# Kernel optimization log

Hardware: AMD Instinct MI355X
Metric: run time of the kernel (lower is better)

Reference implementation:

```python
import jax, jax.numpy as jnp
import numpy as np

D = 1024      # model dim
DH = 64       # dim_head
H = 8         # heads
INNER = DH * H
L = 6         # depth
NL = 64       # num_latents
MF = 128      # max_num_frames
FF = 4 * D    # ff_mult * dim
B, T, F, V = 4, 8, 4, 256


def _ln(x, g, b):
    m = x.mean(-1, keepdims=True)
    v = x.var(-1, keepdims=True)
    return (x - m) / jnp.sqrt(v + 1e-5) * g + b


def setup_inputs() -> dict:
    key = jax.random.key(0)
    ks = jax.random.split(key, 8)
    s = 0.02
    x = jax.random.normal(ks[0], (B, T, F, V, D), jnp.float32)
    latents = jax.random.normal(ks[1], (NL, D), jnp.float32)
    frame_embs = jax.random.normal(ks[2], (MF, D), jnp.float32)
    Wq = jax.random.normal(ks[3], (L, D, INNER), jnp.float32) * s
    Wkv = jax.random.normal(ks[4], (L, D, 2 * INNER), jnp.float32) * s
    Wo = jax.random.normal(ks[5], (L, INNER, D), jnp.float32) * s
    W1 = jax.random.normal(ks[6], (L, D, FF), jnp.float32) * s
    W2 = jax.random.normal(ks[7], (L, FF, D), jnp.float32) * s
    ones = jnp.ones((L, D), jnp.float32)
    zeros = jnp.zeros((L, D), jnp.float32)
    return dict(
        x=x, latents=latents, frame_embs=frame_embs,
        g_media=ones, b_media=zeros, g_lat=ones, b_lat=zeros,
        Wq=Wq, Wkv=Wkv, Wo=Wo, g_ff=ones, b_ff=zeros, W1=W1, W2=W2,
        g_out=jnp.ones((D,), jnp.float32), b_out=jnp.zeros((D,), jnp.float32),
    )


def reference(x, latents, frame_embs, g_media, b_media, g_lat, b_lat,
              Wq, Wkv, Wo, g_ff, b_ff, W1, W2, g_out, b_out):
    scale = DH ** -0.5
    # add frame embeddings (indexed by T, as in original code), merge F,v dims
    x = x + frame_embs[:T][None, :, None, None, :]
    x = x.reshape(B, T, F * V, D)
    lat0 = jnp.broadcast_to(latents, (B, T, NL, D))

    def split_heads(a):  # (b, t, n, h*d) -> (b, h, t, n, d)
        return a.reshape(B, T, -1, H, DH).transpose(0, 3, 1, 2, 4)

    def block(lat, p):
        gm, bm, gl, bl, wq, wkv, wo, gf, bf, w1, w2 = p
        xm = _ln(x, gm, bm)
        ln_l = _ln(lat, gl, bl)
        q = (ln_l @ wq) * scale
        kv = jnp.concatenate([xm, ln_l], axis=-2) @ wkv
        k, v = jnp.split(kv, 2, axis=-1)
        q, k, v = split_heads(q), split_heads(k), split_heads(v)
        sim = jnp.einsum('bhtid,bhtjd->bhtij', q, k)
        attn = jax.nn.softmax(sim, axis=-1)
        o = jnp.einsum('bhtij,bhtjd->bhtid', attn, v)
        o = o.transpose(0, 2, 3, 1, 4).reshape(B, T, NL, INNER)
        lat = o @ wo + lat
        ff = jax.nn.gelu(_ln(lat, gf, bf) @ w1, approximate=False) @ w2
        return lat + ff, None

    lat, _ = jax.lax.scan(block, lat0,
                          (g_media, b_media, g_lat, b_lat, Wq, Wkv, Wo,
                           g_ff, b_ff, W1, W2))
    return _ln(lat, g_out, b_out)
```

## Files before the change

### kernel.cpp

```cpp
#include <hip/hip_runtime.h>
#include <math.h>

#define D_      1024
#define DH_     64
#define H_      8
#define INNER_  512
#define L_      6
#define NL_     64
#define FF_     4096
#define B_      4
#define T_      8
#define FV_     1024
#define BT_     32
#define MROWS_  32768
#define NKV_    1088
#define KVROWS_ 34816
#define ZB_     256

typedef __bf16 bf16;
typedef __bf16 bf16x8 __attribute__((ext_vector_type(8)));
typedef __bf16 bf16x4 __attribute__((ext_vector_type(4)));
typedef float  f32x4  __attribute__((ext_vector_type(4)));

#define BARRIER() { asm volatile("" ::: "memory"); __builtin_amdgcn_s_barrier(); asm volatile("" ::: "memory"); }
#define ENDPH() { __builtin_amdgcn_sched_barrier(0); asm volatile("s_waitcnt lgkmcnt(0)"); __builtin_amdgcn_sched_barrier(0); BARRIER(); }

__device__ __forceinline__ void gload_lds16(const bf16* g, bf16* l) {
    __builtin_amdgcn_global_load_lds(
        (const __attribute__((address_space(1))) unsigned int*)g,
        (__attribute__((address_space(3))) unsigned int*)l, 16, 0, 0);
}

__device__ __forceinline__ float wred_sum(float v) {
#pragma unroll
    for (int o = 32; o > 0; o >>= 1) v += __shfl_xor(v, o, 64);
    return v;
}

__device__ __forceinline__ float gelu_f(float x) {
    return 0.5f * x * (1.0f + erff(x * 0.70710678118654752440f));
}

__global__ __launch_bounds__(256) void xhat_k(const float* __restrict__ x,
                                              const float* __restrict__ fe,
                                              bf16* __restrict__ xhat) {
    __shared__ float red[8];
    int row = blockIdx.x;
    int t = (row >> 10) & 7;
    const float* xr = x + (size_t)row * D_;
    const float* fr_ = fe + (size_t)t * D_;
    int tid = threadIdx.x, c = tid * 4;
    float4 v = *(const float4*)(xr + c);
    float4 f = *(const float4*)(fr_ + c);
    v.x += f.x; v.y += f.y; v.z += f.z; v.w += f.w;
    float s = v.x + v.y + v.z + v.w;
    float ss = v.x * v.x + v.y * v.y + v.z * v.z + v.w * v.w;
    s = wred_sum(s); ss = wred_sum(ss);
    if ((tid & 63) == 0) { red[tid >> 6] = s; red[4 + (tid >> 6)] = ss; }
    __syncthreads();
    s = red[0] + red[1] + red[2] + red[3];
    ss = red[4] + red[5] + red[6] + red[7];
    float mean = s * (1.0f / D_);
    float rstd = rsqrtf(ss * (1.0f / D_) - mean * mean + 1e-5f);
    bf16x4 o;
    o[0] = (bf16)((v.x - mean) * rstd);
    o[1] = (bf16)((v.y - mean) * rstd);
    o[2] = (bf16)((v.z - mean) * rstd);
    o[3] = (bf16)((v.w - mean) * rstd);
    *(bf16x4*)(xhat + (size_t)row * D_ + c) = o;
}

__global__ __launch_bounds__(256) void latinit_k(const float* __restrict__ latents,
                                                 float* __restrict__ lat) {
    int row = blockIdx.x;
    int i = row & 63;
    int c = threadIdx.x * 4;
    float4 v = *(const float4*)(latents + (size_t)i * D_ + c);
    *(float4*)(lat + (size_t)row * D_ + c) = v;
}

template<int OUTF>
__global__ __launch_bounds__(256) void ln_k(const float* __restrict__ in,
                                            const float* __restrict__ g,
                                            const float* __restrict__ b,
                                            void* __restrict__ out) {
    __shared__ float red[8];
    int row = blockIdx.x;
    const float* x = in + (size_t)row * D_;
    int tid = threadIdx.x, c = tid * 4;
    float4 v = *(const float4*)(x + c);
    float s = v.x + v.y + v.z + v.w;
    float ss = v.x * v.x + v.y * v.y + v.z * v.z + v.w * v.w;
    s = wred_sum(s); ss = wred_sum(ss);
    if ((tid & 63) == 0) { red[tid >> 6] = s; red[4 + (tid >> 6)] = ss; }
    __syncthreads();
    s = red[0] + red[1] + red[2] + red[3];
    ss = red[4] + red[5] + red[6] + red[7];
    float mean = s * (1.0f / D_);
    float rstd = rsqrtf(ss * (1.0f / D_) - mean * mean + 1e-5f);
    float4 gv = *(const float4*)(g + c);
    float4 bv = *(const float4*)(b + c);
    float o0 = (v.x - mean) * rstd * gv.x + bv.x;
    float o1 = (v.y - mean) * rstd * gv.y + bv.y;
    float o2 = (v.z - mean) * rstd * gv.z + bv.z;
    float o3 = (v.w - mean) * rstd * gv.w + bv.w;
    if (OUTF) {
        *(float4*)((float*)out + (size_t)row * D_ + c) = make_float4(o0, o1, o2, o3);
    } else {
        bf16x4 o; o[0] = (bf16)o0; o[1] = (bf16)o1; o[2] = (bf16)o2; o[3] = (bf16)o3;
        *(bf16x4*)((bf16*)out + (size_t)row * D_ + c) = o;
    }
}

template<int NP, int OUTF>
__global__ __launch_bounds__(256) void accln_k(float* __restrict__ lat,
                                               const float* __restrict__ p, long long s,
                                               const float* __restrict__ g,
                                               const float* __restrict__ b,
                                               void* __restrict__ out) {
    __shared__ float red[8];
    int row = blockIdx.x;
    int tid = threadIdx.x, c = tid * 4;
    float* lr = lat + (size_t)row * D_;
    float4 a = *(const float4*)(lr + c);
#pragma unroll
    for (int w = 0; w < NP; w++) {
        float4 x = *(const float4*)(p + (size_t)w * s + (size_t)row * D_ + c);
        a.x += x.x; a.y += x.y; a.z += x.z; a.w += x.w;
    }
    if (!OUTF) *(float4*)(lr + c) = a;
    float sm = a.x + a.y + a.z + a.w;
    float ss = a.x * a.x + a.y * a.y + a.z * a.z + a.w * a.w;
    sm = wred_sum(sm); ss = wred_sum(ss);
    if ((tid & 63) == 0) { red[tid >> 6] = sm; red[4 + (tid >> 6)] = ss; }
    __syncthreads();
    sm = red[0] + red[1] + red[2] + red[3];
    ss = red[4] + red[5] + red[6] + red[7];
    float mean = sm * (1.0f / D_);
    float rstd = rsqrtf(ss * (1.0f / D_) - mean * mean + 1e-5f);
    float4 gv = *(const float4*)(g + c);
    float4 bv = *(const float4*)(b + c);
    float o0 = (a.x - mean) * rstd * gv.x + bv.x;
    float o1 = (a.y - mean) * rstd * gv.y + bv.y;
    float o2 = (a.z - mean) * rstd * gv.z + bv.z;
    float o3 = (a.w - mean) * rstd * gv.w + bv.w;
    if (OUTF) {
        *(float4*)((float*)out + (size_t)row * D_ + c) = make_float4(o0, o1, o2, o3);
    } else {
        bf16x4 o; o[0] = (bf16)o0; o[1] = (bf16)o1; o[2] = (bf16)o2; o[3] = (bf16)o3;
        *(bf16x4*)((bf16*)out + (size_t)row * D_ + c) = o;
    }
}

__device__ __forceinline__ void wt_tile(const float* __restrict__ in, int R, int C,
                                        bf16* __restrict__ out, int bx, int by,
                                        const float* __restrict__ sc,
                                        const float* __restrict__ bm,
                                        float* __restrict__ bkv) {
    __shared__ float t[32][33];
    int c0 = bx * 32, r0 = by * 32;
    int tx = threadIdx.x & 31, ty = threadIdx.x >> 5;
#pragma unroll
    for (int i = 0; i < 4; i++)
        t[ty + i * 8][tx] = in[(size_t)(r0 + ty + i * 8) * C + c0 + tx];
    __syncthreads();
    float scale = sc ? sc[r0 + tx] : 1.0f;
#pragma unroll
    for (int i = 0; i < 4; i++)
        out[(size_t)(c0 + ty + i * 8) * R + r0 + tx] = (bf16)(t[tx][ty + i * 8] * scale);
    if (bm && ty == 0) {
        float s = 0.0f;
#pragma unroll
        for (int r = 0; r < 32; r++) s += bm[r0 + r] * t[r][tx];
        atomicAdd(&bkv[c0 + tx], s);
    }
}

__global__ __launch_bounds__(256) void wprep_all(const float* __restrict__ Wq,
                                                 const float* __restrict__ Wkv,
                                                 const float* __restrict__ Wo,
                                                 const float* __restrict__ W1,
                                                 const float* __restrict__ W2,
                                                 const float* __restrict__ g_media,
                                                 const float* __restrict__ b_media,
                                                 float* __restrict__ bkv6,
                                                 bf16* __restrict__ Bcat6,
                                                 bf16* __restrict__ WkvTg6,
                                                 bf16* __restrict__ WoT6,
                                                 bf16* __restrict__ W1T6,
                                                 bf16* __restrict__ W2T6) {
    int l = blockIdx.x / 11264;
    int id = blockIdx.x - l * 11264;
    const float* wq  = Wq + (size_t)l * D_ * INNER_;
    const float* wkv = Wkv + (size_t)l * D_ * 2 * INNER_;
    const float* wo  = Wo + (size_t)l * INNER_ * D_;
    const float* w1  = W1 + (size_t)l * D_ * FF_;
    const float* w2  = W2 + (size_t)l * FF_ * D_;
    bf16* BcatQ  = Bcat6 + (size_t)l * 1536 * D_;
    bf16* BcatKV = BcatQ + (size_t)512 * D_;
    bf16* WkvTg  = WkvTg6 + (size_t)l * D_ * D_;
    bf16* WoT    = WoT6 + (size_t)l * D_ * INNER_;
    bf16* W1T    = W1T6 + (size_t)l * FF_ * D_;
    bf16* W2T    = W2T6 + (size_t)l * D_ * FF_;
    const float* gm = g_media + (size_t)l * D_;
    const float* bm = b_media + (size_t)l * D_;
    float* bkv = bkv6 + (size_t)l * 1024;
    if (id < 512)            wt_tile(wq, D_, INNER_, BcatQ, id & 15, id >> 4, nullptr, nullptr, nullptr);
    else if (id < 1536)  { int i = id - 512;  wt_tile(wkv, D_, 2 * INNER_, BcatKV, i & 31, i >> 5, nullptr, nullptr, nullptr); }
    else if (id < 2560)  { int i = id - 1536; wt_tile(wkv, D_, 2 * INNER_, WkvTg, i & 31, i >> 5, gm, bm, bkv); }
    else if (id < 3072)  { int i = id - 2560; wt_tile(wo, INNER_, D_, WoT, i & 31, i >> 5, nullptr, nullptr, nullptr); }
    else if (id < 7168)  { int i = id - 3072; wt_tile(w1, D_, FF_, W1T, i & 127, i >> 7, nullptr, nullptr, nullptr); }
    else                 { int i = id - 7168; wt_tile(w2, FF_, D_, W2T, i & 31, i >> 5, nullptr, nullptr, nullptr); }
}

__global__ __launch_bounds__(512, 1) void gemm_kv(const bf16* __restrict__ Ag,
                                                  const bf16* __restrict__ Bg,
                                                  bf16* __restrict__ KVb,
                                                  bf16* __restrict__ vt,
                                                  const float* __restrict__ bias) {
    __shared__ bf16 lds[2][32768];
    const int lda = D_, ldb = D_;
    const int tid = threadIdx.x;
    const int w = tid >> 6, lane = tid & 63;
    const int wm = w >> 2, wn = w & 3;
    const size_t m0 = (size_t)blockIdx.x * 256;
    const size_t n0 = (size_t)blockIdx.y * 256;
    const int nt = 16;

    const int p0 = (w * 2) * 64 + lane, p1 = p0 + 64;
    const int sr0 = p0 >> 3, sk0 = ((p0 & 7) ^ (sr0 & 7)) * 8;
    const int sr1 = p1 >> 3, sk1 = ((p1 & 7) ^ (sr1 & 7)) * 8;
    const int scw0 = (w * 2) * 512, scw1 = scw0 + 512;

    auto STAGE = [&](const bf16* g, int ld, size_t row0, int k0, bf16* bufb, int rb) {
        gload_lds16(g + (row0 + sr0) * (size_t)ld + k0 + sk0, bufb + rb + scw0);
        gload_lds16(g + (row0 + sr1) * (size_t)ld + k0 + sk1, bufb + rb + scw1);
    };

    const int fr = lane & 15;
    const int pK0 = (((lane >> 4)) ^ (fr & 7)) * 8;
    const int pK1 = ((4 + (lane >> 4)) ^ (fr & 7)) * 8;
    const size_t aoff = (size_t)(wm * 128 + fr) * 64;
    const size_t boff = 16384 + (size_t)(wn * 64 + fr) * 64;

    f32x4 acc[8][4];
#pragma unroll
    for (int i = 0; i < 8; i++)
#pragma unroll
        for (int j = 0; j < 4; j++)
#pragma unroll
            for (int r = 0; r < 4; r++) acc[i][j][r] = 0.0f;

    STAGE(Bg, ldb, n0,       0, lds[0], 16384);
    STAGE(Bg, ldb, n0 + 128, 0, lds[0], 24576);
    STAGE(Ag, lda, m0,       0, lds[0], 0);
    STAGE(Ag, lda, m0 + 128, 0, lds[0], 8192);
    STAGE(Bg, ldb, n0,       64, lds[1], 16384);
    STAGE(Bg, ldb, n0 + 128, 64, lds[1], 24576);
    STAGE(Ag, lda, m0,       64, lds[1], 0);
    asm volatile("s_waitcnt vmcnt(6)");
    BARRIER();

    for (int t = 0; t < nt; ++t) {
        const bf16* lb = lds[t & 1];
        bf16* lbw = lds[t & 1];
        bf16* lbn = lds[(t + 1) & 1];
        const int kt1 = (t + 1) << 6, kt2 = (t + 2) << 6;
        bf16x8 bfr[4][2];

        {
#pragma unroll
            for (int j = 0; j < 4; j++) {
                bfr[j][0] = *(const bf16x8*)(lb + boff + j * 1024 + pK0);
                bfr[j][1] = *(const bf16x8*)(lb + boff + j * 1024 + pK1);
            }
            bf16x8 a00 = *(const bf16x8*)(lb + aoff + 0 * 1024 + pK0);
            bf16x8 a01 = *(const bf16x8*)(lb + aoff + 0 * 1024 + pK1);
            bf16x8 a10 = *(const bf16x8*)(lb + aoff + 1 * 1024 + pK0);
            bf16x8 a11 = *(const bf16x8*)(lb + aoff + 1 * 1024 + pK1);
            if (t + 1 < nt) STAGE(Ag, lda, m0 + 128, kt1, lbn, 8192);
            BARRIER();
            asm volatile("s_waitcnt lgkmcnt(0)");
            __builtin_amdgcn_s_setprio(1);
#pragma unroll
            for (int j = 0; j < 4; j++) {
                acc[0][j] = __builtin_amdgcn_mfma_f32_16x16x32_bf16(a00, bfr[j][0], acc[0][j], 0, 0, 0);
                acc[0][j] = __builtin_amdgcn_mfma_f32_16x16x32_bf16(a01, bfr[j][1], acc[0][j], 0, 0, 0);
                acc[1][j] = __builtin_amdgcn_mfma_f32_16x16x32_bf16(a10, bfr[j][0], acc[1][j], 0, 0, 0);
                acc[1][j] = __builtin_amdgcn_mfma_f32_16x16x32_bf16(a11, bfr[j][1], acc[1][j], 0, 0, 0);
            }
            __builtin_amdgcn_s_setprio(0);
            BARRIER();
        }
        {
            bf16x8 a00 = *(const bf16x8*)(lb + aoff + 2 * 1024 + pK0);
            bf16x8 a01 = *(const bf16x8*)(lb + aoff + 2 * 1024 + pK1);
            bf16x8 a10 = *(const bf16x8*)(lb + aoff + 3 * 1024 + pK0);
            bf16x8 a11 = *(const bf16x8*)(lb + aoff + 3 * 1024 + pK1);
            if (t + 2 < nt) STAGE(Bg, ldb, n0, kt2, lbw, 16384);
            BARRIER();
            asm volatile("s_waitcnt lgkmcnt(0)");
            __builtin_amdgcn_s_setprio(1);
#pragma unroll
            for (int j = 0; j < 4; j++) {
                acc[2][j] = __builtin_amdgcn_mfma_f32_16x16x32_bf16(a00, bfr[j][0], acc[2][j], 0, 0, 0);
                acc[2][j] = __builtin_amdgcn_mfma_f32_16x16x32_bf16(a01, bfr[j][1], acc[2][j], 0, 0, 0);
                acc[3][j] = __builtin_amdgcn_mfma_f32_16x16x32_bf16(a10, bfr[j][0], acc[3][j], 0, 0, 0);
                acc[3][j] = __builtin_amdgcn_mfma_f32_16x16x32_bf16(a11, bfr[j][1], acc[3][j], 0, 0, 0);
            }
            __builtin_amdgcn_s_setprio(0);
            BARRIER();
        }
        {
            bf16x8 a00 = *(const bf16x8*)(lb + aoff + 4 * 1024 + pK0);
            bf16x8 a01 = *(const bf16x8*)(lb + aoff + 4 * 1024 + pK1);
            bf16x8 a10 = *(const bf16x8*)(lb + aoff + 5 * 1024 + pK0);
            bf16x8 a11 = *(const bf16x8*)(lb + aoff + 5 * 1024 + pK1);
            if (t + 2 < nt) STAGE(Bg, ldb, n0 + 128, kt2, lbw, 24576);
            BARRIER();
            asm volatile("s_waitcnt lgkmcnt(0)");
            __builtin_amdgcn_s_setprio(1);
#pragma unroll
            for (int j = 0; j < 4; j++) {
                acc[4][j] = __builtin_amdgcn_mfma_f32_16x16x32_bf16(a00, bfr[j][0], acc[4][j], 0, 0, 0);
                acc[4][j] = __builtin_amdgcn_mfma_f32_16x16x32_bf16(a01, bfr[j][1], acc[4][j], 0, 0, 0);
                acc[5][j] = __builtin_amdgcn_mfma_f32_16x16x32_bf16(a10, bfr[j][0], acc[5][j], 0, 0, 0);
                acc[5][j] = __builtin_amdgcn_mfma_f32_16x16x32_bf16(a11, bfr[j][1], acc[5][j], 0, 0, 0);
            }
            __builtin_amdgcn_s_setprio(0);
            BARRIER();
        }
        {
            bf16x8 a00 = *(const bf16x8*)(lb + aoff + 6 * 1024 + pK0);
            bf16x8 a01 = *(const bf16x8*)(lb + aoff + 6 * 1024 + pK1);
            bf16x8 a10 = *(const bf16x8*)(lb + aoff + 7 * 1024 + pK0);
            bf16x8 a11 = *(const bf16x8*)(lb + aoff + 7 * 1024 + pK1);
            if (t + 2 < nt) STAGE(Ag, lda, m0, kt2, lbw, 0);
            BARRIER();
            asm volatile("s_waitcnt lgkmcnt(0)");
            __builtin_amdgcn_s_setprio(1);
#pragma unroll
            for (int j = 0; j < 4; j++) {
                acc[6][j] = __builtin_amdgcn_mfma_f32_16x16x32_bf16(a00, bfr[j][0], acc[6][j], 0, 0, 0);
                acc[6][j] = __builtin_amdgcn_mfma_f32_16x16x32_bf16(a01, bfr[j][1], acc[6][j], 0, 0, 0);
                acc[7][j] = __builtin_amdgcn_mfma_f32_16x16x32_bf16(a10, bfr[j][0], acc[7][j], 0, 0, 0);
                acc[7][j] = __builtin_amdgcn_mfma_f32_16x16x32_bf16(a11, bfr[j][1], acc[7][j], 0, 0, 0);
            }
            __builtin_amdgcn_s_setprio(0);
            if (t < nt - 2)       { asm volatile("s_waitcnt vmcnt(6)"); }
            else if (t == nt - 2) { asm volatile("s_waitcnt vmcnt(0)"); }
            BARRIER();
        }
    }

    const int fq = (lane >> 4) * 4;
#pragma unroll
    for (int i = 0; i < 8; i++)
#pragma unroll
        for (int j = 0; j < 4; j++) {
            size_t cb = n0 + wn * 64 + j * 16 + fr;
            float bv = bias[cb];
            size_t mb = m0 + wm * 128 + i * 16 + fq;
            if (cb < 512) {
#pragma unroll
                for (int r = 0; r < 4; r++) {
                    size_t m = mb + r;
                    size_t rb = m + ((m >> 10) << 6);
                    KVb[rb * 512 + cb] = (bf16)(acc[i][j][r] + bv);
                }
            } else {
                int hh = ((int)cb - 512) >> 6, dh = ((int)cb - 512) & 63;
                size_t bt = mb >> 10, jl = mb & 1023;
                bf16x4 v4;
#pragma unroll
                for (int r = 0; r < 4; r++) v4[r] = (bf16)(acc[i][j][r] + bv);
                *(bf16x4*)(vt + ((bt * 8 + hh) * 64 + dh) * (size_t)NKV_ + jl) = v4;
            }
        }
}

template<int MODE>
__global__ __launch_bounds__(512, 1) void gemm_ff(const bf16* __restrict__ Ag, int lda,
                                                  const bf16* __restrict__ Bg, int ldb,
                                                  void* __restrict__ C, int ldc,
                                                  int K, long long czs) {
    __shared__ bf16 lds[2][24576];
    const int tid = threadIdx.x;
    const int w = tid >> 6, lane = tid & 63;
    const int wm = w >> 2, wn = w & 3;
    const size_t m0 = (size_t)blockIdx.x * 128;
    const size_t n0 = (size_t)blockIdx.y * 256;
    const int klen = K / gridDim.z;
    const int koff = blockIdx.z * klen;
    const int nt = klen >> 6;

    const int p0 = (w * 2) * 64 + lane, p1 = p0 + 64;
    const int sr0 = p0 >> 3, sk0 = ((p0 & 7) ^ (sr0 & 7)) * 8;
    const int sr1 = p1 >> 3, sk1 = ((p1 & 7) ^ (sr1 & 7)) * 8;
    const int scw0 = (w * 2) * 512, scw1 = scw0 + 512;

    auto STAGE = [&](const bf16* g, int ld, size_t row0, int k0, bf16* bufb, int rb) {
        gload_lds16(g + (row0 + sr0) * (size_t)ld + k0 + sk0, bufb + rb + scw0);
        gload_lds16(g + (row0 + sr1) * (size_t)ld + k0 + sk1, bufb + rb + scw1);
    };

    const int fr = lane & 15;
    const int pK0 = (((lane >> 4)) ^ (fr & 7)) * 8;
    const int pK1 = ((4 + (lane >> 4)) ^ (fr & 7)) * 8;
    const size_t aoff = (size_t)(wm * 64 + fr) * 64;
    const size_t boff = 8192 + (size_t)(wn * 64 + fr) * 64;

    f32x4 acc[4][4];
#pragma unroll
    for (int i = 0; i < 4; i++)
#pragma unroll
        for (int j = 0; j < 4; j++)
#pragma unroll
            for (int r = 0; r < 4; r++) acc[i][j][r] = 0.0f;

    bf16x8 aX[2], aY[2], bA[4][2], bB[4][2];

    auto LDA1 = [&](const bf16* lb, int i0, bf16x8 (&d)[2]) {
        d[0] = *(const bf16x8*)(lb + aoff + (size_t)i0 * 1024 + pK0);
        d[1] = *(const bf16x8*)(lb + aoff + (size_t)i0 * 1024 + pK1);
    };
    auto LDB8 = [&](const bf16* lb, bf16x8 (&bb)[4][2]) {
#pragma unroll
        for (int j = 0; j < 4; j++) {
            bb[j][0] = *(const bf16x8*)(lb + boff + j * 1024 + pK0);
            bb[j][1] = *(const bf16x8*)(lb + boff + j * 1024 + pK1);
        }
    };
    auto MM1 = [&](int i0, bf16x8 (&a)[2], bf16x8 (&bb)[4][2]) {
        __builtin_amdgcn_s_setprio(1);
#pragma unroll
        for (int j = 0; j < 4; j++) {
            acc[i0][j] = __builtin_amdgcn_mfma_f32_16x16x32_bf16(a[0], bb[j][0], acc[i0][j], 0, 0, 0);
            acc[i0][j] = __builtin_amdgcn_mfma_f32_16x16x32_bf16(a[1], bb[j][1], acc[i0][j], 0, 0, 0);
        }
        __builtin_amdgcn_s_setprio(0);
    };

    STAGE(Ag, lda, m0,       koff,      lds[0], 0);
    STAGE(Bg, ldb, n0,       koff,      lds[0], 8192);
    STAGE(Bg, ldb, n0 + 128, koff,      lds[0], 16384);
    STAGE(Bg, ldb, n0,       koff + 64, lds[1], 8192);
    STAGE(Bg, ldb, n0 + 128, koff + 64, lds[1], 16384);
    asm volatile("s_waitcnt vmcnt(4)");
    BARRIER();
    LDB8(lds[0], bA);
    LDA1(lds[0], 0, aX);

    auto tile4 = [&](const bf16* lb, bf16* lbn, bf16x8 (&BU)[4][2], bf16x8 (&BL)[4][2], int t) {
        bf16* lbw = (bf16*)lb;
        LDA1(lb, 1, aY);
        if (t + 1 < nt) STAGE(Ag, lda, m0, koff + ((t + 1) << 6), lbn, 0);
        MM1(0, aX, BU);
        ENDPH();
        LDA1(lb, 2, aX);
        if (t + 2 < nt) STAGE(Bg, ldb, n0, koff + ((t + 2) << 6), lbw, 8192);
        MM1(1, aY, BU);
        ENDPH();
        LDA1(lb, 3, aY);
        if (t + 2 < nt) STAGE(Bg, ldb, n0 + 128, koff + ((t + 2) << 6), lbw, 16384);
        MM1(2, aX, BU);
        __builtin_amdgcn_sched_barrier(0);
        asm volatile("s_waitcnt lgkmcnt(0)");
        __builtin_amdgcn_sched_barrier(0);
        if (t < nt - 2)       { asm volatile("s_waitcnt vmcnt(4)"); }
        else if (t == nt - 2) { asm volatile("s_waitcnt vmcnt(0)"); }
        BARRIER();
        if (t + 1 < nt) { LDB8(lbn, BL); LDA1(lbn, 0, aX); }
        MM1(3, aY, BU);
        ENDPH();
    };

    for (int t = 0; t < nt; t += 2) {
        tile4(lds[0], lds[1], bA, bB, t);
        tile4(lds[1], lds[0], bB, bA, t + 1);
    }

    const int fq = (lane >> 4) * 4;
#pragma unroll
    for (int i = 0; i < 4; i++)
#pragma unroll
        for (int j = 0; j < 4; j++) {
            size_t cb = n0 + wn * 64 + j * 16 + fr;
            size_t mb = m0 + wm * 64 + i * 16 + fq;
#pragma unroll
            for (int r = 0; r < 4; r++) {
                float v = acc[i][j][r];
                if (MODE == 4) {
                    ((float*)C + blockIdx.z * czs)[(mb + r) * (size_t)ldc + cb] = v;
                } else {
                    ((bf16*)C)[(mb + r) * (size_t)ldc + cb] = (bf16)gelu_f(v);
                }
            }
        }
}

template<int MODE, int CMAP>
__global__ __launch_bounds__(256) void gemm128(const bf16* __restrict__ A, int lda,
                                               const bf16* __restrict__ Bw, int ldb,
                                               void* __restrict__ C, int ldc,
                                               int K, float scale,
                                               long long czs, void* __restrict__ C2,
                                               void* __restrict__ C3) {
    __shared__ bf16 As[128 * 32];
    __shared__ bf16 Bs[128 * 32];
    const int tid = threadIdx.x;
    const int wave = tid >> 6;
    const int lane = tid & 63;
    const size_t m0 = (size_t)blockIdx.x * 128;
    const size_t n0 = (size_t)blockIdx.y * 128;
    const int wm = (wave >> 1) * 64;
    const int wn = (wave & 1) * 64;

    const int klen = K / gridDim.z;
    const int koff = blockIdx.z * klen;

    const int r0 = tid >> 2;
    const int c0 = ((tid & 3) ^ ((tid >> 3) & 3)) * 8;
    const bf16* ga0 = A + (m0 + r0) * lda + c0 + koff;
    const bf16* ga1 = A + (m0 + r0 + 64) * lda + c0 + koff;
    const bf16* gb0 = Bw + (n0 + r0) * ldb + c0 + koff;
    const bf16* gb1 = Bw + (n0 + r0 + 64) * ldb + c0 + koff;
    bf16* la0 = As + wave * 512;
    bf16* la1 = As + 2048 + wave * 512;
    bf16* lb0 = Bs + wave * 512;
    bf16* lb1 = Bs + 2048 + wave * 512;

    f32x4 acc[4][4];
#pragma unroll
    for (int i = 0; i < 4; i++)
#pragma unroll
        for (int j = 0; j < 4; j++)
#pragma unroll
            for (int r = 0; r < 4; r++) acc[i][j][r] = 0.0f;

    const int fr = lane & 15;
    const int q = lane >> 4;
    const int sw = (q ^ ((fr >> 1) & 3)) * 8;

    for (int kt = 0; kt < klen; kt += 32) {
        gload_lds16(ga0 + kt, la0);
        gload_lds16(ga1 + kt, la1);
        gload_lds16(gb0 + kt, lb0);
        gload_lds16(gb1 + kt, lb1);
        __syncthreads();
        bf16x8 af[4], bfv[4];
#pragma unroll
        for (int i = 0; i < 4; i++) {
            af[i]  = *(const bf16x8*)(As + (wm + i * 16 + fr) * 32 + sw);
            bfv[i] = *(const bf16x8*)(Bs + (wn + i * 16 + fr) * 32 + sw);
        }
#pragma unroll
        for (int i = 0; i < 4; i++)
#pragma unroll
            for (int j = 0; j < 4; j++)
                acc[i][j] = __builtin_amdgcn_mfma_f32_16x16x32_bf16(af[i], bfv[j], acc[i][j], 0, 0, 0);
        __syncthreads();
    }

    const int fq = (lane >> 4) * 4;
#pragma unroll
    for (int i = 0; i < 4; i++)
#pragma unroll
        for (int j = 0; j < 4; j++) {
            size_t cb = n0 + wn + j * 16 + fr;
            size_t mb = m0 + wm + i * 16 + fq;
            if (CMAP == 3) {
                if (cb < 512) {
#pragma unroll
                    for (int r = 0; r < 4; r++)
                        ((bf16*)C)[(mb + r) * 512 + cb] = (bf16)(acc[i][j][r] * scale);
                } else if (cb < 1024) {
#pragma unroll
                    for (int r = 0; r < 4; r++) {
                        size_t m = mb + r;
                        size_t rb = (m >> 6) * (size_t)NKV_ + 1024 + (m & 63);
                        ((bf16*)C2)[rb * 512 + (cb - 512)] = (bf16)acc[i][j][r];
                    }
                } else {
                    int hh = ((int)cb - 1024) >> 6, dh = ((int)cb - 1024) & 63;
                    size_t bt = mb >> 6, jl = 1024 + (mb & 63);
                    bf16x4 v4;
#pragma unroll
                    for (int r = 0; r < 4; r++) v4[r] = (bf16)acc[i][j][r];
                    *(bf16x4*)((bf16*)C3 + ((bt * 8 + hh) * 64 + dh) * (size_t)NKV_ + jl) = v4;
                }
            } else {
#pragma unroll
                for (int r = 0; r < 4; r++) {
                    float v = acc[i][j][r];
                    if (MODE == 4) {
                        ((float*)C + blockIdx.z * czs)[(mb + r) * ldc + cb] = v;
                    } else {
                        ((bf16*)C)[(mb + r) * ldc + cb] = (bf16)v;
                    }
                }
            }
        }
}

__global__ __launch_bounds__(256, 2) void attn_k(const bf16* __restrict__ qb,
                                                 const bf16* __restrict__ KVb,
                                                 const bf16* __restrict__ vt,
                                                 float* __restrict__ partO,
                                                 float* __restrict__ partML) {
    __shared__ float comb[4][64 * 66];
    __shared__ float sc[4][64];
    __shared__ float mw[4][64], lw[4][64];
    const int bid = blockIdx.x;
    const int z = bid >> 1, half = bid & 1;
    const int bt = z >> 3, h = z & 7;
    const int tid = threadIdx.x, w = tid >> 6, lane = tid & 63;
    const int fr = lane & 15, g = lane >> 4;
    const bf16* Qz = qb + (size_t)(bt * 64) * INNER_ + h * DH_;
    const bf16* Kz = KVb + (size_t)bt * NKV_ * 512 + h * DH_;
    const bf16* Vz = vt + (size_t)z * (DH_ * NKV_);
    bf16* Pw = (bf16*)(&comb[w][0]);

    bf16x8 qf[4][2];
#pragma unroll
    for (int nj = 0; nj < 4; nj++)
#pragma unroll
        for (int ks = 0; ks < 2; ks++)
            qf[nj][ks] = *(const bf16x8*)(Qz + (size_t)(fr + 16 * nj) * INNER_ + g * 8 + ks * 32);

    f32x4 acc_o[4][4];
#pragma unroll
    for (int i = 0; i < 4; i++)
#pragma unroll
        for (int j = 0; j < 4; j++)
#pragma unroll
            for (int r = 0; r < 4; r++) acc_o[i][j][r] = 0.0f;
    float m_reg[4] = {-INFINITY, -INFINITY, -INFINITY, -INFINITY};
    float l_reg[4] = {0.0f, 0.0f, 0.0f, 0.0f};

    const int cbase = half ? 9 : 0;
    const int nch = half ? 2 : ((w == 0) ? 3 : 2);
    for (int ci = 0; ci < nch; ci++) {
        const int kc0 = (cbase + w + ci * 4) * 64;
        f32x4 s[4][4];
#pragma unroll
        for (int i = 0; i < 4; i++)
#pragma unroll
            for (int j = 0; j < 4; j++)
#pragma unroll
                for (int r = 0; r < 4; r++) s[i][j][r] = 0.0f;
#pragma unroll
        for (int ks = 0; ks < 2; ks++) {
            bf16x8 kf[4];
#pragma unroll
            for (int mi = 0; mi < 4; mi++)
                kf[mi] = *(const bf16x8*)(Kz + (size_t)(kc0 + fr + 16 * mi) * 512 + g * 8 + ks * 32);
#pragma unroll
            for (int mi = 0; mi < 4; mi++)
#pragma unroll
                for (int nj = 0; nj < 4; nj++)
                    s[mi][nj] = __builtin_amdgcn_mfma_f32_16x16x32_bf16(kf[mi], qf[nj][ks], s[mi][nj], 0, 0, 0);
        }
        float pmax[4];
#pragma unroll
        for (int nj = 0; nj < 4; nj++) {
            float mx = s[0][nj][0];
#pragma unroll
            for (int mi = 0; mi < 4; mi++)
#pragma unroll
                for (int r = 0; r < 4; r++) mx = fmaxf(mx, s[mi][nj][r]);
            mx = fmaxf(mx, __shfl_xor(mx, 16, 64));
            mx = fmaxf(mx, __shfl_xor(mx, 32, 64));
            pmax[nj] = mx;
        }
        bool big = (pmax[0] > m_reg[0] + 8.0f) || (pmax[1] > m_reg[1] + 8.0f) ||
                   (pmax[2] > m_reg[2] + 8.0f) || (pmax[3] > m_reg[3] + 8.0f);
        if (__any(big ? 1 : 0)) {
            float so[4];
#pragma unroll
            for (int nj = 0; nj < 4; nj++) {
                float mn = fmaxf(m_reg[nj], pmax[nj]);
                so[nj] = __expf(m_reg[nj] - mn);
                m_reg[nj] = mn;
                l_reg[nj] *= so[nj];
            }
            if (g == 0) {
#pragma unroll
                for (int nj = 0; nj < 4; nj++) sc[w][fr + 16 * nj] = so[nj];
            }
            asm volatile("s_waitcnt lgkmcnt(0)" ::: "memory");
#pragma unroll
            for (int mi = 0; mi < 4; mi++)
#pragma unroll
                for (int r = 0; r < 4; r++) {
                    float sq = sc[w][16 * mi + 4 * g + r];
#pragma unroll
                    for (int jd = 0; jd < 4; jd++) acc_o[mi][jd][r] *= sq;
                }
        }
        float psum[4] = {0.0f, 0.0f, 0.0f, 0.0f};
#pragma unroll
        for (int mi = 0; mi < 4; mi++)
#pragma unroll
            for (int nj = 0; nj < 4; nj++) {
                bf16x4 pb4;
#pragma unroll
                for (int r = 0; r < 4; r++) {
                    float pv = __expf(s[mi][nj][r] - m_reg[nj]);
                    psum[nj] += pv;
                    pb4[r] = (bf16)pv;
                }
                *(bf16x4*)(Pw + (size_t)(fr + 16 * nj) * 72 + 16 * mi + 4 * g) = pb4;
            }
#pragma unroll
        for (int nj = 0; nj < 4; nj++) {
            float ps = psum[nj];
            ps += __shfl_xor(ps, 16, 64);
            ps += __shfl_xor(ps, 32, 64);
            l_reg[nj] += ps;
        }
        asm volatile("s_waitcnt lgkmcnt(0)" ::: "memory");
#pragma unroll
        for (int ks = 0; ks < 2; ks++) {
            bf16x8 af[4], vf[4];
#pragma unroll
            for (int mi = 0; mi < 4; mi++)
                af[mi] = *(const bf16x8*)(Pw + (size_t)(fr + 16 * mi) * 72 + g * 8 + ks * 32);
#pragma unroll
            for (int jd = 0; jd < 4; jd++)
                vf[jd] = *(const bf16x8*)(Vz + (size_t)(fr + 16 * jd) * NKV_ + kc0 + g * 8 + ks * 32);
#pragma unroll
            for (int mi = 0; mi < 4; mi++)
#pragma unroll
                for (int jd = 0; jd < 4; jd++)
                    acc_o[mi][jd] = __builtin_amdgcn_mfma_f32_16x16x32_bf16(af[mi], vf[jd], acc_o[mi][jd], 0, 0, 0);
        }
    }

    if (g == 0) {
#pragma unroll
        for (int nj = 0; nj < 4; nj++) {
            mw[w][fr + 16 * nj] = m_reg[nj];
            lw[w][fr + 16 * nj] = l_reg[nj];
        }
    }
    asm volatile("s_waitcnt lgkmcnt(0)" ::: "memory");
#pragma unroll
    for (int mi = 0; mi < 4; mi++)
#pragma unroll
        for (int jd = 0; jd < 4; jd++)
#pragma unroll
            for (int r = 0; r < 4; r++)
                comb[w][(16 * mi + 4 * g + r) * 66 + fr + 16 * jd] = acc_o[mi][jd][r];
    __syncthreads();
    {
        int q = tid >> 2, d0 = (tid & 3) * 16;
        float M = fmaxf(fmaxf(mw[0][q], mw[1][q]), fmaxf(mw[2][q], mw[3][q]));
        float al[4], l = 0.0f;
#pragma unroll
        for (int ww = 0; ww < 4; ww++) { al[ww] = __expf(mw[ww][q] - M); l += al[ww] * lw[ww][q]; }
        float* pO = partO + (size_t)bid * 4096 + q * 64 + d0;
#pragma unroll
        for (int dd = 0; dd < 16; dd++) {
            float o = 0.0f;
#pragma unroll
            for (int ww = 0; ww < 4; ww++) o += comb[ww][q * 66 + d0 + dd] * al[ww];
            pO[dd] = o;
        }
        if ((tid & 3) == 0) {
            partML[bid * 128 + q] = M;
            partML[bid * 128 + 64 + q] = l;
        }
    }
}

__global__ __launch_bounds__(256) void attn_comb(const float* __restrict__ partO,
                                                 const float* __restrict__ partML,
                                                 bf16* __restrict__ ob) {
    int z = blockIdx.x, bt = z >> 3, h = z & 7;
    int tid = threadIdx.x, q = tid >> 2, d0 = (tid & 3) * 16;
    int b0 = z * 2, b1 = z * 2 + 1;
    float M0 = partML[b0 * 128 + q], l0 = partML[b0 * 128 + 64 + q];
    float M1 = partML[b1 * 128 + q], l1 = partML[b1 * 128 + 64 + q];
    float M = fmaxf(M0, M1);
    float a0 = __expf(M0 - M), a1 = __expf(M1 - M);
    float inv = 1.0f / (a0 * l0 + a1 * l1);
    const float* pO0 = partO + (size_t)b0 * 4096 + q * 64 + d0;
    const float* pO1 = partO + (size_t)b1 * 4096 + q * 64 + d0;
    bf16 outv[16];
#pragma unroll
    for (int dd = 0; dd < 16; dd++)
        outv[dd] = (bf16)((a0 * pO0[dd] + a1 * pO1[dd]) * inv);
    bf16* dst = ob + (size_t)(bt * 64 + q) * INNER_ + h * 64 + d0;
    *(bf16x8*)dst = *(bf16x8*)outv;
    *(bf16x8*)(dst + 8) = *(bf16x8*)(outv + 8);
}

extern "C" void kernel_launch(void* const* d_in, const int* in_sizes, int n_in,
                              void* d_out, int out_size, void* d_ws, size_t ws_size,
                              hipStream_t stream) {
    const float* x       = (const float*)d_in[0];
    const float* latents = (const float*)d_in[1];
    const float* fe      = (const float*)d_in[2];
    const float* g_media = (const float*)d_in[3];
    const float* b_media = (const float*)d_in[4];
    const float* g_lat   = (const float*)d_in[5];
    const float* b_lat   = (const float*)d_in[6];
    const float* Wq      = (const float*)d_in[7];
    const float* Wkv     = (const float*)d_in[8];
    const float* Wo      = (const float*)d_in[9];
    const float* g_ff    = (const float*)d_in[10];
    const float* b_ff    = (const float*)d_in[11];
    const float* W1      = (const float*)d_in[12];
    const float* W2      = (const float*)d_in[13];
    const float* g_out   = (const float*)d_in[14];
    const float* b_out   = (const float*)d_in[15];

    char* p = (char*)d_ws;
    auto alloc = [&](size_t bytes) { char* r = p; p += (bytes + 255) & ~(size_t)255; return r; };
    bf16*  xhat  = (bf16*)alloc((size_t)MROWS_ * D_ * 2);
    float* lat   = (float*)alloc((size_t)2048 * D_ * 4);
    bf16*  lnl   = (bf16*)alloc((size_t)2048 * D_ * 2);
    bf16*  qb    = (bf16*)alloc((size_t)2048 * INNER_ * 2);
    bf16*  KVb   = (bf16*)alloc((size_t)KVROWS_ * 512 * 2);
    bf16*  vt    = (bf16*)alloc((size_t)ZB_ * DH_ * NKV_ * 2);
    bf16*  ob    = (bf16*)alloc((size_t)2048 * INNER_ * 2);
    bf16*  Bcat6 = (bf16*)alloc((size_t)L_ * 1536 * D_ * 2);
    bf16*  WkvTg6= (bf16*)alloc((size_t)L_ * D_ * D_ * 2);
    bf16*  WoT6  = (bf16*)alloc((size_t)L_ * D_ * INNER_ * 2);
    bf16*  W1T6  = (bf16*)alloc((size_t)L_ * FF_ * D_ * 2);
    bf16*  W2T6  = (bf16*)alloc((size_t)L_ * D_ * FF_ * 2);
    float* bkv6  = (float*)alloc((size_t)L_ * 1024 * 4);
    float* ffp   = (float*)alloc((size_t)4 * 2048 * D_ * 4);
    bf16*  ffh   = vt;
    float* partO = ffp;
    float* partML= ffp + (size_t)512 * 4096;

    xhat_k<<<MROWS_, 256, 0, stream>>>(x, fe, xhat);
    latinit_k<<<2048, 256, 0, stream>>>(latents, lat);
    ln_k<0><<<2048, 256, 0, stream>>>(lat, g_lat, b_lat, lnl);
    hipMemsetAsync(bkv6, 0, (size_t)L_ * 1024 * 4, stream);
    wprep_all<<<L_ * 11264, 256, 0, stream>>>(Wq, Wkv, Wo, W1, W2, g_media, b_media,
                                              bkv6, Bcat6, WkvTg6, WoT6, W1T6, W2T6);

    const long long PS = (long long)2048 * D_;

    for (int l = 0; l < L_; l++) {
        const float* gf = g_ff + (size_t)l * D_;
        const float* bf_ = b_ff + (size_t)l * D_;
        bf16* Bcat  = Bcat6 + (size_t)l * 1536 * D_;
        bf16* WkvTg = WkvTg6 + (size_t)l * D_ * D_;
        bf16* WoT   = WoT6 + (size_t)l * D_ * INNER_;
        bf16* W1T   = W1T6 + (size_t)l * FF_ * D_;
        bf16* W2T   = W2T6 + (size_t)l * D_ * FF_;
        float* bkv  = bkv6 + (size_t)l * 1024;

        gemm_kv<<<dim3(128, 4), 512, 0, stream>>>(xhat, WkvTg, KVb, vt, bkv);
        gemm128<0, 3><<<dim3(16, 12), 256, 0, stream>>>(
            lnl, D_, Bcat, D_, qb, 0, D_, 0.125f, 0, KVb, vt);

        attn_k<<<2 * ZB_, 256, 0, stream>>>(qb, KVb, vt, partO, partML);
        attn_comb<<<ZB_, 256, 0, stream>>>(partO, partML, ob);

        gemm128<4, 0><<<dim3(16, 8, 2), 256, 0, stream>>>(
            ob, INNER_, WoT, INNER_, ffp, D_, INNER_, 1.0f, PS, nullptr, nullptr);
        accln_k<2, 0><<<2048, 256, 0, stream>>>(lat, ffp, PS, gf, bf_, lnl);

        gemm_ff<3><<<dim3(16, 16), 512, 0, stream>>>(
            lnl, D_, W1T, D_, ffh, FF_, D_, 0);
        gemm_ff<4><<<dim3(16, 4, 4), 512, 0, stream>>>(
            ffh, FF_, W2T, FF_, ffp, D_, FF_, PS);
        if (l < L_ - 1) {
            accln_k<4, 0><<<2048, 256, 0, stream>>>(lat, ffp, PS,
                g_lat + (size_t)(l + 1) * D_, b_lat + (size_t)(l + 1) * D_, lnl);
        } else {
            accln_k<4, 1><<<2048, 256, 0, stream>>>(lat, ffp, PS, g_out, b_out, (float*)d_out);
        }
    }
}
```

Before: 1.330 ms.

## Merge split-KV attention into single pass and use 64x64 weight-transpose tiles

The attention kernel no longer splits each (bt,h) across two blocks with a separate combine kernel. Each block now walks all 17 KV chunks across its four waves and normalises and writes bf16 output directly, which removes the partial-output round trip through global memory and one launch per layer. The price is half as many blocks (256) for attention, so fewer CUs are busy. Separately, the weight-prep transpose goes from 32x32 to 64x64 tiles, which cuts the block count fourfold but uses more LDS per block.

```diff
diff --git a/kernel.cpp b/kernel.cpp
--- a/kernel.cpp
+++ b/kernel.cpp
@@ -152,26 +152,26 @@
     }
 }
 
-__device__ __forceinline__ void wt_tile(const float* __restrict__ in, int R, int C,
-                                        bf16* __restrict__ out, int bx, int by,
-                                        const float* __restrict__ sc,
-                                        const float* __restrict__ bm,
-                                        float* __restrict__ bkv) {
-    __shared__ float t[32][33];
-    int c0 = bx * 32, r0 = by * 32;
-    int tx = threadIdx.x & 31, ty = threadIdx.x >> 5;
-#pragma unroll
-    for (int i = 0; i < 4; i++)
-        t[ty + i * 8][tx] = in[(size_t)(r0 + ty + i * 8) * C + c0 + tx];
+__device__ __forceinline__ void wt_tile64(const float* __restrict__ in, int R, int C,
+                                          bf16* __restrict__ out, int bx, int by,
+                                          const float* __restrict__ sc,
+                                          const float* __restrict__ bm,
+                                          float* __restrict__ bkv) {
+    __shared__ float t[64][65];
+    int c0 = bx * 64, r0 = by * 64;
+    int tx = threadIdx.x & 63, ty = threadIdx.x >> 6;
+#pragma unroll
+    for (int i = 0; i < 16; i++)
+        t[ty + i * 4][tx] = in[(size_t)(r0 + ty + i * 4) * C + c0 + tx];
     __syncthreads();
     float scale = sc ? sc[r0 + tx] : 1.0f;
 #pragma unroll
-    for (int i = 0; i < 4; i++)
-        out[(size_t)(c0 + ty + i * 8) * R + r0 + tx] = (bf16)(t[tx][ty + i * 8] * scale);
+    for (int i = 0; i < 16; i++)
+        out[(size_t)(c0 + ty + i * 4) * R + r0 + tx] = (bf16)(t[tx][ty + i * 4] * scale);
     if (bm && ty == 0) {
         float s = 0.0f;
 #pragma unroll
-        for (int r = 0; r < 32; r++) s += bm[r0 + r] * t[r][tx];
+        for (int r = 0; r < 64; r++) s += bm[r0 + r] * t[r][tx];
         atomicAdd(&bkv[c0 + tx], s);
     }
 }
@@ -189,8 +189,8 @@
                                                  bf16* __restrict__ WoT6,
                                                  bf16* __restrict__ W1T6,
                                                  bf16* __restrict__ W2T6) {
-    int l = blockIdx.x / 11264;
-    int id = blockIdx.x - l * 11264;
+    int l = blockIdx.x / 2816;
+    int id = blockIdx.x - l * 2816;
     const float* wq  = Wq + (size_t)l * D_ * INNER_;
     const float* wkv = Wkv + (size_t)l * D_ * 2 * INNER_;
     const float* wo  = Wo + (size_t)l * INNER_ * D_;
@@ -205,12 +205,12 @@
     const float* gm = g_media + (size_t)l * D_;
     const float* bm = b_media + (size_t)l * D_;
     float* bkv = bkv6 + (size_t)l * 1024;
-    if (id < 512)            wt_tile(wq, D_, INNER_, BcatQ, id & 15, id >> 4, nullptr, nullptr, nullptr);
-    else if (id < 1536)  { int i = id - 512;  wt_tile(wkv, D_, 2 * INNER_, BcatKV, i & 31, i >> 5, nullptr, nullptr, nullptr); }
-    else if (id < 2560)  { int i = id - 1536; wt_tile(wkv, D_, 2 * INNER_, WkvTg, i & 31, i >> 5, gm, bm, bkv); }
-    else if (id < 3072)  { int i = id - 2560; wt_tile(wo, INNER_, D_, WoT, i & 31, i >> 5, nullptr, nullptr, nullptr); }
-    else if (id < 7168)  { int i = id - 3072; wt_tile(w1, D_, FF_, W1T, i & 127, i >> 7, nullptr, nullptr, nullptr); }
-    else                 { int i = id - 7168; wt_tile(w2, FF_, D_, W2T, i & 31, i >> 5, nullptr, nullptr, nullptr); }
+    if (id < 128)            wt_tile64(wq, D_, INNER_, BcatQ, id & 7, id >> 3, nullptr, nullptr, nullptr);
+    else if (id < 384)   { int i = id - 128;  wt_tile64(wkv, D_, 2 * INNER_, BcatKV, i & 15, i >> 4, nullptr, nullptr, nullptr); }
+    else if (id < 640)   { int i = id - 384;  wt_tile64(wkv, D_, 2 * INNER_, WkvTg, i & 15, i >> 4, gm, bm, bkv); }
+    else if (id < 768)   { int i = id - 640;  wt_tile64(wo, INNER_, D_, WoT, i & 15, i >> 4, nullptr, nullptr, nullptr); }
+    else if (id < 1792)  { int i = id - 768;  wt_tile64(w1, D_, FF_, W1T, i & 63, i >> 6, nullptr, nullptr, nullptr); }
+    else                 { int i = id - 1792; wt_tile64(w2, FF_, D_, W2T, i & 15, i >> 4, nullptr, nullptr, nullptr); }
 }
 
 __global__ __launch_bounds__(512, 1) void gemm_kv(const bf16* __restrict__ Ag,
@@ -606,14 +606,11 @@
 __global__ __launch_bounds__(256, 2) void attn_k(const bf16* __restrict__ qb,
                                                  const bf16* __restrict__ KVb,
                                                  const bf16* __restrict__ vt,
-                                                 float* __restrict__ partO,
-                                                 float* __restrict__ partML) {
+                                                 bf16* __restrict__ ob) {
     __shared__ float comb[4][64 * 66];
     __shared__ float sc[4][64];
     __shared__ float mw[4][64], lw[4][64];
-    const int bid = blockIdx.x;
-    const int z = bid >> 1, half = bid & 1;
-    const int bt = z >> 3, h = z & 7;
+    const int z = blockIdx.x, bt = z >> 3, h = z & 7;
     const int tid = threadIdx.x, w = tid >> 6, lane = tid & 63;
     const int fr = lane & 15, g = lane >> 4;
     const bf16* Qz = qb + (size_t)(bt * 64) * INNER_ + h * DH_;
@@ -638,10 +635,9 @@
     float m_reg[4] = {-INFINITY, -INFINITY, -INFINITY, -INFINITY};
     float l_reg[4] = {0.0f, 0.0f, 0.0f, 0.0f};
 
-    const int cbase = half ? 9 : 0;
-    const int nch = half ? 2 : ((w == 0) ? 3 : 2);
+    const int nch = (w == 0) ? 5 : 4;
     for (int ci = 0; ci < nch; ci++) {
-        const int kc0 = (cbase + w + ci * 4) * 64;
+        const int kc0 = (w + ci * 4) * 64;
         f32x4 s[4][4];
 #pragma unroll
         for (int i = 0; i < 4; i++)
@@ -759,41 +755,19 @@
         float al[4], l = 0.0f;
 #pragma unroll
         for (int ww = 0; ww < 4; ww++) { al[ww] = __expf(mw[ww][q] - M); l += al[ww] * lw[ww][q]; }
-        float* pO = partO + (size_t)bid * 4096 + q * 64 + d0;
+        float inv = 1.0f / l;
+        bf16 outv[16];
 #pragma unroll
         for (int dd = 0; dd < 16; dd++) {
             float o = 0.0f;
 #pragma unroll
             for (int ww = 0; ww < 4; ww++) o += comb[ww][q * 66 + d0 + dd] * al[ww];
-            pO[dd] = o;
-        }
-        if ((tid & 3) == 0) {
-            partML[bid * 128 + q] = M;
-            partML[bid * 128 + 64 + q] = l;
-        }
-    }
-}
-
-__global__ __launch_bounds__(256) void attn_comb(const float* __restrict__ partO,
-                                                 const float* __restrict__ partML,
-                                                 bf16* __restrict__ ob) {
-    int z = blockIdx.x, bt = z >> 3, h = z & 7;
-    int tid = threadIdx.x, q = tid >> 2, d0 = (tid & 3) * 16;
-    int b0 = z * 2, b1 = z * 2 + 1;
-    float M0 = partML[b0 * 128 + q], l0 = partML[b0 * 128 + 64 + q];
-    float M1 = partML[b1 * 128 + q], l1 = partML[b1 * 128 + 64 + q];
-    float M = fmaxf(M0, M1);
-    float a0 = __expf(M0 - M), a1 = __expf(M1 - M);
-    float inv = 1.0f / (a0 * l0 + a1 * l1);
-    const float* pO0 = partO + (size_t)b0 * 4096 + q * 64 + d0;
-    const float* pO1 = partO + (size_t)b1 * 4096 + q * 64 + d0;
-    bf16 outv[16];
-#pragma unroll
-    for (int dd = 0; dd < 16; dd++)
-        outv[dd] = (bf16)((a0 * pO0[dd] + a1 * pO1[dd]) * inv);
-    bf16* dst = ob + (size_t)(bt * 64 + q) * INNER_ + h * 64 + d0;
-    *(bf16x8*)dst = *(bf16x8*)outv;
-    *(bf16x8*)(dst + 8) = *(bf16x8*)(outv + 8);
+            outv[dd] = (bf16)(o * inv);
+        }
+        bf16* dst = ob + (size_t)(bt * 64 + q) * INNER_ + h * 64 + d0;
+        *(bf16x8*)dst = *(bf16x8*)outv;
+        *(bf16x8*)(dst + 8) = *(bf16x8*)(outv + 8);
+    }
 }
 
 extern "C" void kernel_launch(void* const* d_in, const int* in_sizes, int n_in,
@@ -833,15 +807,13 @@
     float* bkv6  = (float*)alloc((size_t)L_ * 1024 * 4);
     float* ffp   = (float*)alloc((size_t)4 * 2048 * D_ * 4);
     bf16*  ffh   = vt;
-    float* partO = ffp;
-    float* partML= ffp + (size_t)512 * 4096;
 
     xhat_k<<<MROWS_, 256, 0, stream>>>(x, fe, xhat);
     latinit_k<<<2048, 256, 0, stream>>>(latents, lat);
     ln_k<0><<<2048, 256, 0, stream>>>(lat, g_lat, b_lat, lnl);
     hipMemsetAsync(bkv6, 0, (size_t)L_ * 1024 * 4, stream);
-    wprep_all<<<L_ * 11264, 256, 0, stream>>>(Wq, Wkv, Wo, W1, W2, g_media, b_media,
-                                              bkv6, Bcat6, WkvTg6, WoT6, W1T6, W2T6);
+    wprep_all<<<L_ * 2816, 256, 0, stream>>>(Wq, Wkv, Wo, W1, W2, g_media, b_media,
+                                             bkv6, Bcat6, WkvTg6, WoT6, W1T6, W2T6);
 
     const long long PS = (long long)2048 * D_;
 
@@ -859,8 +831,7 @@
         gemm128<0, 3><<<dim3(16, 12), 256, 0, stream>>>(
             lnl, D_, Bcat, D_, qb, 0, D_, 0.125f, 0, KVb, vt);
 
-        attn_k<<<2 * ZB_, 256, 0, stream>>>(qb, KVb, vt, partO, partML);
-        attn_comb<<<ZB_, 256, 0, stream>>>(partO, partML, ob);
+        attn_k<<<ZB_, 256, 0, stream>>>(qb, KVb, vt, ob);
 
         gemm128<4, 0><<<dim3(16, 8, 2), 256, 0, stream>>>(
             ob, INNER_, WoT, INNER_, ffp, D_, INNER_, 1.0f, PS, nullptr, nullptr);
```

Result: faster. 1.296 ms (-2.5%).
